# Optimization experiments

Measured on AMD Instinct MI355X. Metric: run time of the kernel, lower is better.

Reference implementation:

```python
import jax, jax.numpy as jnp
import numpy as np


def _fft_conv(x, filts):
    # x: [B, inC, S, S] real; filts: [inC, outC, k, k, 2] (real/imag channels)
    # Matches FFT_Conv_Layer: zero-pad bottom/right by k-1, FFT, complex
    # multiply-accumulate over inC, inverse FFT, crop [1:-1, 1:-1], take real.
    N = x.shape[-1] + filts.shape[-2] - 1  # imgSize + filtSize - 1
    Fx = jnp.fft.fft2(x, s=(N, N))                      # [B, inC, N, N] complex
    fc = filts[..., 0] + 1j * filts[..., 1]             # [inC, outC, k, k] complex
    Ff = jnp.fft.fft2(fc, s=(N, N))                     # [inC, outC, N, N]
    prod = jnp.einsum('bihw,iohw->bohw', Fx, Ff)        # sum over inC, no huge 5D temp
    return jnp.real(jnp.fft.ifft2(prod))[:, :, 1:-1, 1:-1]


def _spectral_pool(x, fsize):
    # Keep lowest `fsize` frequencies (corner crop of the FFT), inverse FFT, ReLU.
    F = jnp.fft.fft2(x)
    n = (fsize - 1) // 2
    tl = F[:, :, :n + 1, :n + 1]
    tr = F[:, :, :n + 1, -n:]
    bl = F[:, :, -n:, :n + 1]
    br = F[:, :, -n:, -n:]
    top = jnp.concatenate([tl, tr], axis=-1)
    bot = jnp.concatenate([bl, br], axis=-1)
    out = jnp.real(jnp.fft.ifft2(jnp.concatenate([top, bot], axis=-2)))
    return jax.nn.relu(out)


def setup_inputs() -> dict:
    key = jax.random.key(0)
    ks = jax.random.split(key, 10)
    B = 16
    filt_shapes = [(3, 32), (32, 64), (64, 128), (128, 256), (256, 256)]
    inp = {'x': jax.random.normal(ks[0], (B, 3, 224, 224), dtype=jnp.float32)}
    for i, (ci, co) in enumerate(filt_shapes):
        inp[f'f{i + 1}'] = 0.01 * jax.random.normal(ks[1 + i], (ci, co, 3, 3, 2), dtype=jnp.float32)
    inp['gamma'] = jnp.ones((256,), jnp.float32)
    inp['beta'] = jnp.zeros((256,), jnp.float32)
    inp['W1'] = 0.02 * jax.random.normal(ks[6], (9216, 512), dtype=jnp.float32)
    inp['b1'] = jnp.zeros((512,), jnp.float32)
    inp['W2'] = 0.02 * jax.random.normal(ks[7], (512, 256), dtype=jnp.float32)
    inp['b2'] = jnp.zeros((256,), jnp.float32)
    inp['W3'] = 0.02 * jax.random.normal(ks[8], (256, 10), dtype=jnp.float32)
    inp['b3'] = jnp.zeros((10,), jnp.float32)
    return inp


def reference(x, f1, f2, f3, f4, f5, gamma, beta, W1, b1, W2, b2, W3, b3):
    h = _spectral_pool(_fft_conv(x, f1), 113)   # [B, 32, 113, 113]
    h = _spectral_pool(_fft_conv(h, f2), 55)    # [B, 64, 55, 55]
    h = _spectral_pool(_fft_conv(h, f3), 27)    # [B, 128, 27, 27]
    h = _spectral_pool(_fft_conv(h, f4), 13)    # [B, 256, 13, 13]
    h = _fft_conv(h, f5)                        # [B, 256, 13, 13]
    # BatchNorm2d (training mode: batch statistics, biased variance)
    mean = jnp.mean(h, axis=(0, 2, 3), keepdims=True)
    var = jnp.var(h, axis=(0, 2, 3), keepdims=True)
    h = (h - mean) * jax.lax.rsqrt(var + 1e-5)
    h = h * gamma.reshape(1, -1, 1, 1) + beta.reshape(1, -1, 1, 1)
    # AdaptiveAvgPool2d((6,6)) on 13x13 == avg pool, kernel 3, stride 2
    h = jax.lax.reduce_window(h, 0.0, jax.lax.add, (1, 1, 3, 3), (1, 1, 2, 2), 'VALID') / 9.0
    h = h.reshape(h.shape[0], -1)               # [B, 9216]
    # dropout omitted (deterministic reference)
    h = jax.nn.relu(h @ W1 + b1)
    h = jax.nn.relu(h @ W2 + b2)
    return jax.nn.log_softmax(h @ W3 + b3, axis=1)
```

## Files before the change

### kernel.cpp

```cpp
#include <hip/hip_runtime.h>
#include <hip/hip_bf16.h>

typedef __attribute__((ext_vector_type(8))) short short8_t;
typedef __attribute__((ext_vector_type(4))) float float4_t;

#define OFF_CF  0u
#define OFF_PB1 25690112u
#define OFF_PB2 38765568u
#define OFF_PB3 44960768u
#define OFF_PB4 47946752u
#define OFF_C5  49331200u
#define OFF_AP  52100096u
#define OFF_H1  52689920u
#define OFF_H2  52722688u
#define OFF_P   52739072u
#define OFF_FPK 53918720u
#define OFF_PPK 55890944u

static __device__ __forceinline__ unsigned short f2bf(float v) {
    __hip_bfloat16 h = __float2bfloat16(v);
    return *(unsigned short*)&h;
}
static __device__ __forceinline__ float bf2f(unsigned short u) {
    __hip_bfloat16 h = *(__hip_bfloat16*)&u;
    return __bfloat162float(h);
}
static __device__ __forceinline__ unsigned short ld_bf(const float* p) { return f2bf(*p); }
static __device__ __forceinline__ unsigned short ld_bf(const unsigned short* p) { return *p; }
static __device__ __forceinline__ void st_out(float* p, float v) { *p = v; }
static __device__ __forceinline__ void st_out(unsigned short* p, float v) { *p = f2bf(v); }

__global__ void pack_f_k(const float* __restrict__ f, unsigned short* __restrict__ A,
                         int Ci, int Co, int CIR) {
    int id = blockIdx.x * 256 + threadIdx.x;
    int nci = Ci >> 5;
    int total = (Co >> 4) * nci * 9 * 512;
    if (id >= total) return;
    int j = id & 7, lane = (id >> 3) & 63;
    int uv = (id >> 9) % 9;
    int rest = id / (512 * 9);
    int cc = rest % nci, co_blk = rest / nci;
    int m = lane & 15, k = ((lane >> 4) << 3) + j;
    int ci = (cc << 5) + k, co = (co_blk << 4) + m;
    float v = (ci < CIR) ? f[((size_t)(ci * Co + co) * 9 + uv) * 2] : 0.f;
    A[id] = f2bf(v);
}

__global__ void pack_pool_k(unsigned short* __restrict__ P, int M, int N, int RT, int KC) {
    int id = blockIdx.x * 256 + threadIdx.x;
    if (id >= RT * KC * 512) return;
    int j = id & 7, lane = (id >> 3) & 63;
    int c = (id >> 9) % KC, rt = id / (512 * KC);
    int row = (rt << 4) + (lane & 15);
    int col = (c << 5) + ((lane >> 4) << 3) + j;
    double val = 0.0;
    if (row < M && col < N) {
        int n = (M - 1) / 2;
        double w = 6.283185307179586476925286766559 *
                   ((double)row / (double)M - (double)col / (double)N);
        double acc = 1.0;
        for (int a = 1; a <= n; ++a) acc += 2.0 * cos(w * (double)a);
        val = acc / (double)M;
    }
    float vf = (float)val;
    unsigned short hi = f2bf(vf);
    unsigned short lo = f2bf(vf - bf2f(hi));
    size_t base = ((size_t)(rt * KC + c) * 2) * 512 + lane * 8 + j;
    P[base] = hi;
    P[base + 512] = lo;
}

template<int CI, int CIR, int CO, int COB, int PBLK, int WQT, typename Tin, typename Tout>
__global__ __launch_bounds__(256) void conv_mfma2_k(const Tin* __restrict__ x,
        const unsigned short* __restrict__ Apk, Tout* __restrict__ y, int H) {
    constexpr int ROWS = PBLK + 2;
    constexpr int QW = WQT * 16 + 2;
    constexpr int RC = ROWS * QW;
    constexpr int NCC = CI >> 5;
    constexpr int NCOG = CO / COB;
    constexpr int NC = (WQT == 2) ? (COB / 32) : (COB / 64);
    __shared__ unsigned short xs[RC * 40];
    int b = blockIdx.z / NCOG;
    int co0 = (blockIdx.z % NCOG) * COB;
    int q0 = blockIdx.x * (WQT * 16);
    int p0 = blockIdx.y * PBLK;
    int tid = threadIdx.x;
    int lane = tid & 63, w = tid >> 6;
    int l15 = lane & 15;
    int kch = lane >> 4;
    int mg = kch << 2;
    int qt = (WQT == 2) ? (w & 1) : 0;
    int ctb = (WQT == 2) ? ((w >> 1) * NC) : (w * NC);
    const Tin* xb = x + (size_t)b * CIR * H * H;
    float4_t acc[PBLK][NC];
#pragma unroll
    for (int pr = 0; pr < PBLK; ++pr)
#pragma unroll
        for (int nc = 0; nc < NC; ++nc) acc[pr][nc] = (float4_t){0.f, 0.f, 0.f, 0.f};
    for (int cc = 0; cc < NCC; ++cc) {
        for (int i = tid; i < RC * 32; i += 256) {
            int ci = i / RC;
            int rc = i - ci * RC;
            int r = rc / QW;
            int c = rc - r * QW;
            int gp = p0 - 1 + r, gq = q0 - 1 + c;
            unsigned short v = 0;
            if ((CI == CIR || ((cc << 5) + ci) < CIR) &&
                (unsigned)gp < (unsigned)H && (unsigned)gq < (unsigned)H)
                v = ld_bf(&xb[((size_t)((cc << 5) + ci) * H + gp) * H + gq]);
            xs[rc * 40 + ((((ci >> 3) ^ ((rc >> 3) & 3)) << 3) | (ci & 7))] = v;
        }
        __syncthreads();
#pragma unroll
        for (int uv = 0; uv < 9; ++uv) {
            const int u = uv / 3, v = uv % 3;
            short8_t af[NC];
#pragma unroll
            for (int nc = 0; nc < NC; ++nc) {
                int ct = (co0 >> 4) + ctb + nc;
                af[nc] = *(const short8_t*)(Apk +
                    (((size_t)ct * NCC + cc) * 9 + uv) * 512 + lane * 8);
            }
#pragma unroll
            for (int pr = 0; pr < PBLK; ++pr) {
                int rcL = (pr + 2 - u) * QW + qt * 16 + (2 - v) + l15;
                int addr = rcL * 40 + ((kch ^ ((rcL >> 3) & 3)) << 3);
                short8_t bf = *(const short8_t*)(&xs[addr]);
#pragma unroll
                for (int nc = 0; nc < NC; ++nc)
                    acc[pr][nc] = __builtin_amdgcn_mfma_f32_16x16x32_bf16(
                        af[nc], bf, acc[pr][nc], 0, 0, 0);
            }
        }
        __syncthreads();
    }
    int q = q0 + qt * 16 + l15;
    if (q < H) {
#pragma unroll
        for (int pr = 0; pr < PBLK; ++pr) {
            int p = p0 + pr;
            if (p < H) {
#pragma unroll
                for (int nc = 0; nc < NC; ++nc) {
                    Tout* yb = y + (((size_t)b * CO + co0 + (ctb + nc) * 16 + mg) * H + p) * H + q;
#pragma unroll
                    for (int r2 = 0; r2 < 4; ++r2)
                        st_out(&yb[(size_t)r2 * H * H], acc[pr][nc][r2]);
                }
            }
        }
    }
}

template<int N, int M, int TRT>
__global__ __launch_bounds__(256) void pool_mfma_k(const float* __restrict__ x,
                                                   const unsigned short* __restrict__ PK,
                                                   unsigned short* __restrict__ out) {
    constexpr int MT = (N + 15) / 16;
    constexpr int RT = (M + 15) / 16;
    constexpr int KC = (N + 31) / 32;
    constexpr int XPAD = 40;
    constexpr int ZPAD = KC * 32 + 8;
    constexpr int XROWS = MT * 16;
    constexpr int NT1 = MT * TRT;
    constexpr int L1 = (NT1 + 3) / 4;
    constexpr int NT2 = RT * TRT;
    constexpr int L2 = (NT2 + 3) / 4;
    __shared__ unsigned short xh[XROWS * XPAD], xl[XROWS * XPAD];
    __shared__ unsigned short zh[16 * TRT * ZPAD], zl[16 * TRT * ZPAD];

    int t0g = blockIdx.x * TRT;
    int bc = blockIdx.y;
    int tid = threadIdx.x;
    int lane = tid & 63, w = tid >> 6;
    int l15 = lane & 15;
    int kb = (lane >> 4) << 3;
    const float* xb = x + (size_t)bc * N * N;

    float4_t acc[L1];
#pragma unroll
    for (int i = 0; i < L1; ++i) acc[i] = (float4_t){0.f, 0.f, 0.f, 0.f};

    for (int c = 0; c < KC; ++c) {
        for (int id = tid; id < XROWS * 32; id += 256) {
            int u = id >> 5, vv = id & 31, v = (c << 5) + vv;
            float val = (u < N && v < N) ? xb[u * N + v] : 0.f;
            unsigned short hi = f2bf(val);
            xh[u * XPAD + vv] = hi;
            xl[u * XPAD + vv] = f2bf(val - bf2f(hi));
        }
        __syncthreads();
#pragma unroll
        for (int li = 0; li < L1; ++li) {
            int idx = li * 4 + w;
            if (idx < NT1) {
                int mt = idx / TRT, nt = idx % TRT;
                short8_t ahi = *(const short8_t*)(&xh[(mt * 16 + l15) * XPAD + kb]);
                short8_t alo = *(const short8_t*)(&xl[(mt * 16 + l15) * XPAD + kb]);
                const unsigned short* bp =
                    PK + ((size_t)((t0g + nt) * KC + c) * 2) * 512 + lane * 8;
                short8_t bhi = *(const short8_t*)bp;
                short8_t blo = *(const short8_t*)(bp + 512);
                acc[li] = __builtin_amdgcn_mfma_f32_16x16x32_bf16(ahi, bhi, acc[li], 0, 0, 0);
                acc[li] = __builtin_amdgcn_mfma_f32_16x16x32_bf16(ahi, blo, acc[li], 0, 0, 0);
                acc[li] = __builtin_amdgcn_mfma_f32_16x16x32_bf16(alo, bhi, acc[li], 0, 0, 0);
            }
        }
        __syncthreads();
    }
#pragma unroll
    for (int li = 0; li < L1; ++li) {
        int idx = li * 4 + w;
        if (idx < NT1) {
            int mt = idx / TRT, nt = idx % TRT;
            int t = nt * 16 + l15;
            int u0 = mt * 16 + ((lane >> 4) << 2);
            unsigned short h0 = f2bf(acc[li][0]), h1 = f2bf(acc[li][1]);
            unsigned short h2 = f2bf(acc[li][2]), h3 = f2bf(acc[li][3]);
            unsigned long long ph =
                (unsigned long long)h0 | ((unsigned long long)h1 << 16) |
                ((unsigned long long)h2 << 32) | ((unsigned long long)h3 << 48);
            unsigned long long pl =
                (unsigned long long)f2bf(acc[li][0] - bf2f(h0)) |
                ((unsigned long long)f2bf(acc[li][1] - bf2f(h1)) << 16) |
                ((unsigned long long)f2bf(acc[li][2] - bf2f(h2)) << 32) |
                ((unsigned long long)f2bf(acc[li][3] - bf2f(h3)) << 48);
            *(unsigned long long*)(&zh[t * ZPAD + u0]) = ph;
            *(unsigned long long*)(&zl[t * ZPAD + u0]) = pl;
        }
    }
    __syncthreads();

    float4_t acc2[L2];
#pragma unroll
    for (int i = 0; i < L2; ++i) acc2[i] = (float4_t){0.f, 0.f, 0.f, 0.f};
    for (int c = 0; c < KC; ++c) {
#pragma unroll
        for (int li = 0; li < L2; ++li) {
            int idx = li * 4 + w;
            if (idx < NT2) {
                int mt = idx / TRT, nt = idx % TRT;
                const unsigned short* ap =
                    PK + ((size_t)(mt * KC + c) * 2) * 512 + lane * 8;
                short8_t ahi = *(const short8_t*)ap;
                short8_t alo = *(const short8_t*)(ap + 512);
                short8_t bzh = *(const short8_t*)(&zh[(nt * 16 + l15) * ZPAD + (c << 5) + kb]);
                short8_t bzl = *(const short8_t*)(&zl[(nt * 16 + l15) * ZPAD + (c << 5) + kb]);
                acc2[li] = __builtin_amdgcn_mfma_f32_16x16x32_bf16(ahi, bzh, acc2[li], 0, 0, 0);
                acc2[li] = __builtin_amdgcn_mfma_f32_16x16x32_bf16(ahi, bzl, acc2[li], 0, 0, 0);
                acc2[li] = __builtin_amdgcn_mfma_f32_16x16x32_bf16(alo, bzh, acc2[li], 0, 0, 0);
            }
        }
    }
    unsigned short* ob = out + (size_t)bc * M * M;
#pragma unroll
    for (int li = 0; li < L2; ++li) {
        int idx = li * 4 + w;
        if (idx < NT2) {
            int mt = idx / TRT, nt = idx % TRT;
            int t = (t0g + nt) * 16 + l15;
            if (t < M) {
                int s0 = mt * 16 + ((lane >> 4) << 2);
#pragma unroll
                for (int r = 0; r < 4; ++r) {
                    int s = s0 + r;
                    if (s < M) ob[s * M + t] = f2bf(fmaxf(acc2[li][r], 0.f));
                }
            }
        }
    }
}

__global__ void bn_k(float* __restrict__ h, const float* __restrict__ gamma,
                     const float* __restrict__ beta) {
    int c = blockIdx.x;
    int tid = threadIdx.x;
    float s = 0.f, s2 = 0.f;
    for (int i = tid; i < 16 * 169; i += 256) {
        int b = i / 169, hw = i % 169;
        float v = h[((size_t)b * 256 + c) * 169 + hw];
        s += v; s2 += v * v;
    }
    __shared__ float red[256], red2[256];
    red[tid] = s; red2[tid] = s2;
    __syncthreads();
    for (int st = 128; st > 0; st >>= 1) {
        if (tid < st) { red[tid] += red[tid + st]; red2[tid] += red2[tid + st]; }
        __syncthreads();
    }
    __shared__ float sc, sh;
    if (tid == 0) {
        float mean = red[0] / (16.f * 169.f);
        float var  = red2[0] / (16.f * 169.f) - mean * mean;
        float inv  = rsqrtf(var + 1e-5f);
        sc = gamma[c] * inv;
        sh = beta[c] - mean * sc;
    }
    __syncthreads();
    for (int i = tid; i < 16 * 169; i += 256) {
        int b = i / 169, hw = i % 169;
        size_t idx = ((size_t)b * 256 + c) * 169 + hw;
        h[idx] = h[idx] * sc + sh;
    }
}

__global__ void avgpool_k(const float* __restrict__ h, float* __restrict__ ap) {
    int id = blockIdx.x * 256 + threadIdx.x;
    if (id >= 16 * 256 * 36) return;
    int j = id % 6, i = (id / 6) % 6, c = (id / 36) % 256, b = id / (36 * 256);
    const float* hb = h + ((size_t)b * 256 + c) * 169;
    float s = 0.f;
#pragma unroll
    for (int di = 0; di < 3; ++di)
#pragma unroll
        for (int dj = 0; dj < 3; ++dj)
            s += hb[(2 * i + di) * 13 + (2 * j + dj)];
    ap[(size_t)b * 9216 + c * 36 + i * 6 + j] = s * (1.f / 9.f);
}

template<int BATCH, int KLEN>
__global__ void fc_part_k(const float* __restrict__ h, const float* __restrict__ W,
                          float* __restrict__ P, int Kdim, int N) {
    __shared__ float hs[BATCH * KLEN];
    __shared__ float red[BATCH * 64];
    int tx = threadIdx.x, ty = threadIdx.y;
    int tid = ty * 64 + tx;
    int o = blockIdx.x * 64 + tx;
    int k0 = blockIdx.y * KLEN;
    for (int i = tid; i < BATCH * KLEN; i += 256) {
        int b = i / KLEN, k = i % KLEN;
        hs[i] = h[(size_t)b * Kdim + k0 + k];
    }
    __syncthreads();
    float acc[BATCH];
#pragma unroll
    for (int b = 0; b < BATCH; ++b) acc[b] = 0.f;
    for (int k = ty; k < KLEN; k += 4) {
        float w = W[(size_t)(k0 + k) * N + o];
#pragma unroll
        for (int b = 0; b < BATCH; ++b) acc[b] += hs[b * KLEN + k] * w;
    }
    for (int kz = 0; kz < 4; ++kz) {
        if (ty == kz) {
#pragma unroll
            for (int b = 0; b < BATCH; ++b) {
                if (kz == 0) red[b * 64 + tx] = acc[b];
                else         red[b * 64 + tx] += acc[b];
            }
        }
        __syncthreads();
    }
    if (ty == 0) {
#pragma unroll
        for (int b = 0; b < BATCH; ++b)
            P[((size_t)blockIdx.y * BATCH + b) * N + o] = red[b * 64 + tx];
    }
}

template<int BATCH>
__global__ void fc_reduce_k(const float* __restrict__ P, const float* __restrict__ bias,
                            float* __restrict__ out, int N, int KS, int relu) {
    int id = blockIdx.x * 256 + threadIdx.x;
    if (id >= BATCH * N) return;
    int b = id / N, o = id % N;
    float s = bias[o];
    for (int ks = 0; ks < KS; ++ks) s += P[((size_t)ks * BATCH + b) * N + o];
    if (relu) s = fmaxf(s, 0.f);
    out[(size_t)b * N + o] = s;
}

__global__ void fc3_softmax_k(const float* __restrict__ h, const float* __restrict__ W,
                              const float* __restrict__ bias, float* __restrict__ out) {
    int b = blockIdx.x;
    int o = threadIdx.x;
    __shared__ float l[10];
    if (o < 10) {
        float acc = bias[o];
        for (int k = 0; k < 256; ++k) acc += h[b * 256 + k] * W[k * 10 + o];
        l[o] = acc;
    }
    __syncthreads();
    if (o == 0) {
        float m = l[0];
        for (int i = 1; i < 10; ++i) m = fmaxf(m, l[i]);
        float s = 0.f;
        for (int i = 0; i < 10; ++i) s += expf(l[i] - m);
        float lse = m + logf(s);
        for (int i = 0; i < 10; ++i) out[b * 10 + i] = l[i] - lse;
    }
}

extern "C" void kernel_launch(void* const* d_in, const int* in_sizes, int n_in,
                              void* d_out, int out_size, void* d_ws, size_t ws_size,
                              hipStream_t stream) {
    const float* x     = (const float*)d_in[0];
    const float* f1    = (const float*)d_in[1];
    const float* f2    = (const float*)d_in[2];
    const float* f3    = (const float*)d_in[3];
    const float* f4    = (const float*)d_in[4];
    const float* f5    = (const float*)d_in[5];
    const float* gamma = (const float*)d_in[6];
    const float* beta  = (const float*)d_in[7];
    const float* W1    = (const float*)d_in[8];
    const float* b1    = (const float*)d_in[9];
    const float* W2    = (const float*)d_in[10];
    const float* b2    = (const float*)d_in[11];
    const float* W3    = (const float*)d_in[12];
    const float* b3    = (const float*)d_in[13];
    float* out = (float*)d_out;
    char* ws = (char*)d_ws;

    float* CF = (float*)(ws + OFF_CF);
    unsigned short* PB1 = (unsigned short*)(ws + OFF_PB1);
    unsigned short* PB2 = (unsigned short*)(ws + OFF_PB2);
    unsigned short* PB3 = (unsigned short*)(ws + OFF_PB3);
    unsigned short* PB4 = (unsigned short*)(ws + OFF_PB4);
    float* C5 = (float*)(ws + OFF_C5);
    float* AP = (float*)(ws + OFF_AP);
    float* H1 = (float*)(ws + OFF_H1);
    float* H2 = (float*)(ws + OFF_H2);
    float* P  = (float*)(ws + OFF_P);
    unsigned short* PK1 = (unsigned short*)(ws + OFF_FPK);
    unsigned short* PK2 = PK1 + 9216;
    unsigned short* PK3 = PK2 + 18432;
    unsigned short* PK4 = PK3 + 73728;
    unsigned short* PK5 = PK4 + 294912;
    unsigned short* PP1 = (unsigned short*)(ws + OFF_PPK);
    unsigned short* PP2 = PP1 + 57344;
    unsigned short* PP3 = PP2 + 16384;
    unsigned short* PP4 = PP3 + 4096;

    pack_f_k<<<36,   256, 0, stream>>>(f1, PK1, 32, 32, 3);
    pack_f_k<<<72,   256, 0, stream>>>(f2, PK2, 32, 64, 32);
    pack_f_k<<<288,  256, 0, stream>>>(f3, PK3, 64, 128, 64);
    pack_f_k<<<1152, 256, 0, stream>>>(f4, PK4, 128, 256, 128);
    pack_f_k<<<2304, 256, 0, stream>>>(f5, PK5, 256, 256, 256);
    pack_pool_k<<<(8 * 7 * 512 + 255) / 256, 256, 0, stream>>>(PP1, 113, 224, 8, 7);
    pack_pool_k<<<(4 * 4 * 512 + 255) / 256, 256, 0, stream>>>(PP2, 55, 113, 4, 4);
    pack_pool_k<<<(2 * 2 * 512 + 255) / 256, 256, 0, stream>>>(PP3, 27, 55, 2, 2);
    pack_pool_k<<<(1 * 1 * 512 + 255) / 256, 256, 0, stream>>>(PP4, 13, 27, 1, 1);

    for (int ck = 0; ck < 4; ++ck) {
        int b0 = ck * 4;
        conv_mfma2_k<32, 3, 32, 32, 6, 2, float, float>
            <<<dim3(7, 38, 4), 256, 0, stream>>>(x + (size_t)b0 * 3 * 224 * 224, PK1, CF, 224);
        pool_mfma_k<224, 113, 4><<<dim3(2, 4 * 32), 256, 0, stream>>>(
            CF, PP1, PB1 + (size_t)b0 * 32 * 113 * 113);
    }
    for (int ck = 0; ck < 4; ++ck) {
        int b0 = ck * 4;
        conv_mfma2_k<32, 32, 64, 64, 6, 2, unsigned short, float>
            <<<dim3(4, 19, 4), 256, 0, stream>>>(PB1 + (size_t)b0 * 32 * 113 * 113, PK2, CF, 113);
        pool_mfma_k<113, 55, 4><<<dim3(1, 4 * 64), 256, 0, stream>>>(
            CF, PP2, PB2 + (size_t)b0 * 64 * 55 * 55);
    }
    conv_mfma2_k<64, 64, 128, 128, 6, 2, unsigned short, float>
        <<<dim3(2, 10, 16), 256, 0, stream>>>(PB2, PK3, CF, 55);
    pool_mfma_k<55, 27, 2><<<dim3(1, 16 * 128), 256, 0, stream>>>(CF, PP3, PB3);
    conv_mfma2_k<128, 128, 256, 128, 4, 2, unsigned short, float>
        <<<dim3(1, 7, 32), 256, 0, stream>>>(PB3, PK4, CF, 27);
    pool_mfma_k<27, 13, 1><<<dim3(1, 16 * 256), 256, 0, stream>>>(CF, PP4, PB4);
    conv_mfma2_k<256, 256, 256, 128, 2, 1, unsigned short, float>
        <<<dim3(1, 7, 32), 256, 0, stream>>>(PB4, PK5, C5, 13);

    bn_k<<<256, 256, 0, stream>>>(C5, gamma, beta);
    avgpool_k<<<(16 * 256 * 36 + 255) / 256, 256, 0, stream>>>(C5, AP);
    fc_part_k<16, 256><<<dim3(512 / 64, 36), dim3(64, 4), 0, stream>>>(AP, W1, P, 9216, 512);
    fc_reduce_k<16><<<(16 * 512 + 255) / 256, 256, 0, stream>>>(P, b1, H1, 512, 36, 1);
    fc_part_k<16, 64><<<dim3(256 / 64, 8), dim3(64, 4), 0, stream>>>(H1, W2, P, 512, 256);
    fc_reduce_k<16><<<(16 * 256 + 255) / 256, 256, 0, stream>>>(P, b2, H2, 256, 8, 1);
    fc3_softmax_k<<<16, 64, 0, stream>>>(H2, W3, b3, out);
}
```

Baseline: 777.7 us.

## Vectorize conv input staging with padded row strides and merge small kernels

```diff
diff --git a/kernel.cpp b/kernel.cpp
--- a/kernel.cpp
+++ b/kernel.cpp
@@ -5,17 +5,17 @@
 typedef __attribute__((ext_vector_type(4))) float float4_t;
 
 #define OFF_CF  0u
-#define OFF_PB1 25690112u
-#define OFF_PB2 38765568u
-#define OFF_PB3 44960768u
-#define OFF_PB4 47946752u
-#define OFF_C5  49331200u
-#define OFF_AP  52100096u
-#define OFF_H1  52689920u
-#define OFF_H2  52722688u
-#define OFF_P   52739072u
-#define OFF_FPK 53918720u
-#define OFF_PPK 55890944u
+#define OFF_PB1 26214400u
+#define OFF_PB2 40099840u
+#define OFF_PB3 46407680u
+#define OFF_PB4 49946624u
+#define OFF_C5  51650560u
+#define OFF_AP  54419456u
+#define OFF_H1  55009280u
+#define OFF_H2  55042048u
+#define OFF_P   55058432u
+#define OFF_FPK 56238080u
+#define OFF_PPK 58210304u
 
 static __device__ __forceinline__ unsigned short f2bf(float v) {
     __hip_bfloat16 h = __float2bfloat16(v);
@@ -27,15 +27,21 @@
 }
 static __device__ __forceinline__ unsigned short ld_bf(const float* p) { return f2bf(*p); }
 static __device__ __forceinline__ unsigned short ld_bf(const unsigned short* p) { return *p; }
-static __device__ __forceinline__ void st_out(float* p, float v) { *p = v; }
-static __device__ __forceinline__ void st_out(unsigned short* p, float v) { *p = f2bf(v); }
-
-__global__ void pack_f_k(const float* __restrict__ f, unsigned short* __restrict__ A,
-                         int Ci, int Co, int CIR) {
-    int id = blockIdx.x * 256 + threadIdx.x;
+
+__global__ void pack_f_all(const float* f1, const float* f2, const float* f3,
+                           const float* f4, const float* f5,
+                           unsigned short* A1, unsigned short* A2, unsigned short* A3,
+                           unsigned short* A4, unsigned short* A5) {
+    int bx = blockIdx.x;
+    const float* f; unsigned short* A; int Ci, Co, CIR, base;
+    if (bx < 36)        { f = f1; A = A1; Ci = 32;  Co = 32;  CIR = 3;   base = 0; }
+    else if (bx < 108)  { f = f2; A = A2; Ci = 32;  Co = 64;  CIR = 32;  base = 36; }
+    else if (bx < 396)  { f = f3; A = A3; Ci = 64;  Co = 128; CIR = 64;  base = 108; }
+    else if (bx < 1548) { f = f4; A = A4; Ci = 128; Co = 256; CIR = 128; base = 396; }
+    else                { f = f5; A = A5; Ci = 256; Co = 256; CIR = 256; base = 1548; }
+    int id = (bx - base) * 256 + threadIdx.x;
     int nci = Ci >> 5;
-    int total = (Co >> 4) * nci * 9 * 512;
-    if (id >= total) return;
+    if (id >= (Co >> 4) * nci * 9 * 512) return;
     int j = id & 7, lane = (id >> 3) & 63;
     int uv = (id >> 9) % 9;
     int rest = id / (512 * 9);
@@ -46,8 +52,16 @@
     A[id] = f2bf(v);
 }
 
-__global__ void pack_pool_k(unsigned short* __restrict__ P, int M, int N, int RT, int KC) {
-    int id = blockIdx.x * 256 + threadIdx.x;
+__global__ void pack_pool_all(unsigned short* P1, unsigned short* P2,
+                              unsigned short* P3, unsigned short* P4) {
+    int bx = blockIdx.x;
+    unsigned short* P; int M, N, KC, base;
+    if (bx < 112)      { P = P1; M = 113; N = 224; KC = 7; base = 0; }
+    else if (bx < 144) { P = P2; M = 55;  N = 113; KC = 4; base = 112; }
+    else if (bx < 152) { P = P3; M = 27;  N = 55;  KC = 2; base = 144; }
+    else               { P = P4; M = 13;  N = 27;  KC = 1; base = 152; }
+    int id = (bx - base) * 256 + threadIdx.x;
+    int RT = (M + 15) / 16;
     if (id >= RT * KC * 512) return;
     int j = id & 7, lane = (id >> 3) & 63;
     int c = (id >> 9) % KC, rt = id / (512 * KC);
@@ -65,16 +79,17 @@
     float vf = (float)val;
     unsigned short hi = f2bf(vf);
     unsigned short lo = f2bf(vf - bf2f(hi));
-    size_t base = ((size_t)(rt * KC + c) * 2) * 512 + lane * 8 + j;
-    P[base] = hi;
-    P[base + 512] = lo;
-}
-
-template<int CI, int CIR, int CO, int COB, int PBLK, int WQT, typename Tin, typename Tout>
-__global__ __launch_bounds__(256) void conv_mfma2_k(const Tin* __restrict__ x,
-        const unsigned short* __restrict__ Apk, Tout* __restrict__ y, int H) {
+    size_t bo = ((size_t)(rt * KC + c) * 2) * 512 + lane * 8 + j;
+    P[bo] = hi;
+    P[bo + 512] = lo;
+}
+
+template<int CI, int CIR, int CO, int COB, int PBLK, int WQT, typename Tin>
+__global__ __launch_bounds__(256) void conv_mfma3_k(const Tin* __restrict__ x,
+        const unsigned short* __restrict__ Apk, float* __restrict__ y, int H, int HS) {
     constexpr int ROWS = PBLK + 2;
     constexpr int QW = WQT * 16 + 2;
+    constexpr int QCH8 = (QW + 14) / 8;
     constexpr int RC = ROWS * QW;
     constexpr int NCC = CI >> 5;
     constexpr int NCOG = CO / COB;
@@ -91,24 +106,52 @@
     int mg = kch << 2;
     int qt = (WQT == 2) ? (w & 1) : 0;
     int ctb = (WQT == 2) ? ((w >> 1) * NC) : (w * NC);
-    const Tin* xb = x + (size_t)b * CIR * H * H;
+    const Tin* xb = x + (size_t)b * CIR * H * HS;
     float4_t acc[PBLK][NC];
 #pragma unroll
     for (int pr = 0; pr < PBLK; ++pr)
 #pragma unroll
         for (int nc = 0; nc < NC; ++nc) acc[pr][nc] = (float4_t){0.f, 0.f, 0.f, 0.f};
     for (int cc = 0; cc < NCC; ++cc) {
-        for (int i = tid; i < RC * 32; i += 256) {
-            int ci = i / RC;
-            int rc = i - ci * RC;
-            int r = rc / QW;
-            int c = rc - r * QW;
-            int gp = p0 - 1 + r, gq = q0 - 1 + c;
-            unsigned short v = 0;
-            if ((CI == CIR || ((cc << 5) + ci) < CIR) &&
-                (unsigned)gp < (unsigned)H && (unsigned)gq < (unsigned)H)
-                v = ld_bf(&xb[((size_t)((cc << 5) + ci) * H + gp) * H + gq]);
-            xs[rc * 40 + ((((ci >> 3) ^ ((rc >> 3) & 3)) << 3) | (ci & 7))] = v;
+        for (int i = tid; i < 32 * ROWS * QCH8; i += 256) {
+            int ci = i / (ROWS * QCH8);
+            int rem = i - ci * (ROWS * QCH8);
+            int r = rem / QCH8, ch = rem - r * QCH8;
+            int gci = (cc << 5) + ci;
+            int gp = p0 - 1 + r;
+            int gq0 = q0 - 8 + ch * 8;
+            bool rowok = (CI == CIR || gci < CIR) && ((unsigned)gp < (unsigned)H);
+            unsigned short vv[8];
+            if (rowok && ch >= 1 && ch * 8 <= QW - 1 && gq0 >= 0 && gq0 + 7 < H) {
+                const Tin* src = &xb[((size_t)gci * H + gp) * HS + gq0];
+                if constexpr (sizeof(Tin) == 2) {
+                    short8_t v8 = *(const short8_t*)src;
+#pragma unroll
+                    for (int j = 0; j < 8; ++j) vv[j] = (unsigned short)v8[j];
+                } else {
+                    float4_t f0 = *(const float4_t*)src;
+                    float4_t g0 = *(const float4_t*)(src + 4);
+#pragma unroll
+                    for (int j = 0; j < 4; ++j) { vv[j] = f2bf(f0[j]); vv[4 + j] = f2bf(g0[j]); }
+                }
+            } else {
+#pragma unroll
+                for (int j = 0; j < 8; ++j) {
+                    int gq = gq0 + j;
+                    unsigned short u = 0;
+                    if (rowok && (unsigned)gq < (unsigned)H)
+                        u = ld_bf(&xb[((size_t)gci * H + gp) * HS + gq]);
+                    vv[j] = u;
+                }
+            }
+#pragma unroll
+            for (int j = 0; j < 8; ++j) {
+                int c8 = ch * 8 + j - 7;
+                if ((unsigned)c8 < (unsigned)QW) {
+                    int rc = r * QW + c8;
+                    xs[rc * 40 + ((((ci >> 3) ^ ((rc >> 3) & 3)) << 3) | (ci & 7))] = vv[j];
+                }
+            }
         }
         __syncthreads();
 #pragma unroll
@@ -142,17 +185,17 @@
             if (p < H) {
 #pragma unroll
                 for (int nc = 0; nc < NC; ++nc) {
-                    Tout* yb = y + (((size_t)b * CO + co0 + (ctb + nc) * 16 + mg) * H + p) * H + q;
+                    float* yb = y + (((size_t)b * CO + co0 + (ctb + nc) * 16 + mg) * H + p) * H + q;
 #pragma unroll
                     for (int r2 = 0; r2 < 4; ++r2)
-                        st_out(&yb[(size_t)r2 * H * H], acc[pr][nc][r2]);
+                        yb[(size_t)r2 * H * H] = acc[pr][nc][r2];
                 }
             }
         }
     }
 }
 
-template<int N, int M, int TRT>
+template<int N, int M, int TRT, int MS>
 __global__ __launch_bounds__(256) void pool_mfma_k(const float* __restrict__ x,
                                                    const unsigned short* __restrict__ PK,
                                                    unsigned short* __restrict__ out) {
@@ -252,7 +295,7 @@
             }
         }
     }
-    unsigned short* ob = out + (size_t)bc * M * M;
+    unsigned short* ob = out + (size_t)bc * M * MS;
 #pragma unroll
     for (int li = 0; li < L2; ++li) {
         int idx = li * 4 + w;
@@ -264,24 +307,25 @@
 #pragma unroll
                 for (int r = 0; r < 4; ++r) {
                     int s = s0 + r;
-                    if (s < M) ob[s * M + t] = f2bf(fmaxf(acc2[li][r], 0.f));
+                    if (s < M) ob[s * MS + t] = f2bf(fmaxf(acc2[li][r], 0.f));
                 }
             }
         }
     }
 }
 
-__global__ void bn_k(float* __restrict__ h, const float* __restrict__ gamma,
-                     const float* __restrict__ beta) {
-    int c = blockIdx.x;
-    int tid = threadIdx.x;
+__global__ __launch_bounds__(256) void bn_avgpool_k(const float* __restrict__ h,
+        const float* __restrict__ gamma, const float* __restrict__ beta,
+        float* __restrict__ ap) {
+    int c = blockIdx.x, tid = threadIdx.x;
+    __shared__ float hs[16 * 169];
+    __shared__ float red[256], red2[256];
     float s = 0.f, s2 = 0.f;
     for (int i = tid; i < 16 * 169; i += 256) {
         int b = i / 169, hw = i % 169;
         float v = h[((size_t)b * 256 + c) * 169 + hw];
-        s += v; s2 += v * v;
-    }
-    __shared__ float red[256], red2[256];
+        hs[i] = v; s += v; s2 += v * v;
+    }
     red[tid] = s; red2[tid] = s2;
     __syncthreads();
     for (int st = 128; st > 0; st >>= 1) {
@@ -297,25 +341,17 @@
         sh = beta[c] - mean * sc;
     }
     __syncthreads();
-    for (int i = tid; i < 16 * 169; i += 256) {
-        int b = i / 169, hw = i % 169;
-        size_t idx = ((size_t)b * 256 + c) * 169 + hw;
-        h[idx] = h[idx] * sc + sh;
-    }
-}
-
-__global__ void avgpool_k(const float* __restrict__ h, float* __restrict__ ap) {
-    int id = blockIdx.x * 256 + threadIdx.x;
-    if (id >= 16 * 256 * 36) return;
-    int j = id % 6, i = (id / 6) % 6, c = (id / 36) % 256, b = id / (36 * 256);
-    const float* hb = h + ((size_t)b * 256 + c) * 169;
-    float s = 0.f;
-#pragma unroll
-    for (int di = 0; di < 3; ++di)
-#pragma unroll
-        for (int dj = 0; dj < 3; ++dj)
-            s += hb[(2 * i + di) * 13 + (2 * j + dj)];
-    ap[(size_t)b * 9216 + c * 36 + i * 6 + j] = s * (1.f / 9.f);
+    for (int i = tid; i < 16 * 36; i += 256) {
+        int b = i / 36, r = i % 36, ii = r / 6, jj = r % 6;
+        const float* hb = &hs[b * 169];
+        float sum = 0.f;
+#pragma unroll
+        for (int di = 0; di < 3; ++di)
+#pragma unroll
+            for (int dj = 0; dj < 3; ++dj)
+                sum += hb[(2 * ii + di) * 13 + 2 * jj + dj];
+        ap[(size_t)b * 9216 + c * 36 + r] = sum * (1.f / 9.f) * sc + sh;
+    }
 }
 
 template<int BATCH, int KLEN>
@@ -430,41 +466,33 @@
     unsigned short* PP3 = PP2 + 16384;
     unsigned short* PP4 = PP3 + 4096;
 
-    pack_f_k<<<36,   256, 0, stream>>>(f1, PK1, 32, 32, 3);
-    pack_f_k<<<72,   256, 0, stream>>>(f2, PK2, 32, 64, 32);
-    pack_f_k<<<288,  256, 0, stream>>>(f3, PK3, 64, 128, 64);
-    pack_f_k<<<1152, 256, 0, stream>>>(f4, PK4, 128, 256, 128);
-    pack_f_k<<<2304, 256, 0, stream>>>(f5, PK5, 256, 256, 256);
-    pack_pool_k<<<(8 * 7 * 512 + 255) / 256, 256, 0, stream>>>(PP1, 113, 224, 8, 7);
-    pack_pool_k<<<(4 * 4 * 512 + 255) / 256, 256, 0, stream>>>(PP2, 55, 113, 4, 4);
-    pack_pool_k<<<(2 * 2 * 512 + 255) / 256, 256, 0, stream>>>(PP3, 27, 55, 2, 2);
-    pack_pool_k<<<(1 * 1 * 512 + 255) / 256, 256, 0, stream>>>(PP4, 13, 27, 1, 1);
+    pack_f_all<<<3852, 256, 0, stream>>>(f1, f2, f3, f4, f5, PK1, PK2, PK3, PK4, PK5);
+    pack_pool_all<<<154, 256, 0, stream>>>(PP1, PP2, PP3, PP4);
 
     for (int ck = 0; ck < 4; ++ck) {
         int b0 = ck * 4;
-        conv_mfma2_k<32, 3, 32, 32, 6, 2, float, float>
-            <<<dim3(7, 38, 4), 256, 0, stream>>>(x + (size_t)b0 * 3 * 224 * 224, PK1, CF, 224);
-        pool_mfma_k<224, 113, 4><<<dim3(2, 4 * 32), 256, 0, stream>>>(
-            CF, PP1, PB1 + (size_t)b0 * 32 * 113 * 113);
-    }
-    for (int ck = 0; ck < 4; ++ck) {
-        int b0 = ck * 4;
-        conv_mfma2_k<32, 32, 64, 64, 6, 2, unsigned short, float>
-            <<<dim3(4, 19, 4), 256, 0, stream>>>(PB1 + (size_t)b0 * 32 * 113 * 113, PK2, CF, 113);
-        pool_mfma_k<113, 55, 4><<<dim3(1, 4 * 64), 256, 0, stream>>>(
-            CF, PP2, PB2 + (size_t)b0 * 64 * 55 * 55);
-    }
-    conv_mfma2_k<64, 64, 128, 128, 6, 2, unsigned short, float>
-        <<<dim3(2, 10, 16), 256, 0, stream>>>(PB2, PK3, CF, 55);
-    pool_mfma_k<55, 27, 2><<<dim3(1, 16 * 128), 256, 0, stream>>>(CF, PP3, PB3);
-    conv_mfma2_k<128, 128, 256, 128, 4, 2, unsigned short, float>
-        <<<dim3(1, 7, 32), 256, 0, stream>>>(PB3, PK4, CF, 27);
-    pool_mfma_k<27, 13, 1><<<dim3(1, 16 * 256), 256, 0, stream>>>(CF, PP4, PB4);
-    conv_mfma2_k<256, 256, 256, 128, 2, 1, unsigned short, float>
-        <<<dim3(1, 7, 32), 256, 0, stream>>>(PB4, PK5, C5, 13);
-
-    bn_k<<<256, 256, 0, stream>>>(C5, gamma, beta);
-    avgpool_k<<<(16 * 256 * 36 + 255) / 256, 256, 0, stream>>>(C5, AP);
+        conv_mfma3_k<32, 3, 32, 32, 6, 2, float>
+            <<<dim3(7, 38, 4), 256, 0, stream>>>(x + (size_t)b0 * 3 * 224 * 224, PK1, CF, 224, 224);
+        pool_mfma_k<224, 113, 4, 120><<<dim3(2, 4 * 32), 256, 0, stream>>>(
+            CF, PP1, PB1 + (size_t)b0 * 32 * 113 * 120);
+    }
+    for (int ck = 0; ck < 2; ++ck) {
+        int b0 = ck * 8;
+        conv_mfma3_k<32, 32, 64, 64, 6, 2, unsigned short>
+            <<<dim3(4, 19, 8), 256, 0, stream>>>(PB1 + (size_t)b0 * 32 * 113 * 120, PK2, CF, 113, 120);
+        pool_mfma_k<113, 55, 4, 56><<<dim3(1, 8 * 64), 256, 0, stream>>>(
+            CF, PP2, PB2 + (size_t)b0 * 64 * 55 * 56);
+    }
+    conv_mfma3_k<64, 64, 128, 64, 6, 2, unsigned short>
+        <<<dim3(2, 10, 32), 256, 0, stream>>>(PB2, PK3, CF, 55, 56);
+    pool_mfma_k<55, 27, 2, 32><<<dim3(1, 16 * 128), 256, 0, stream>>>(CF, PP3, PB3);
+    conv_mfma3_k<128, 128, 256, 64, 4, 2, unsigned short>
+        <<<dim3(1, 7, 64), 256, 0, stream>>>(PB3, PK4, CF, 27, 32);
+    pool_mfma_k<27, 13, 1, 16><<<dim3(1, 16 * 256), 256, 0, stream>>>(CF, PP4, PB4);
+    conv_mfma3_k<256, 256, 256, 64, 2, 1, unsigned short>
+        <<<dim3(1, 7, 64), 256, 0, stream>>>(PB4, PK5, C5, 13, 16);
+
+    bn_avgpool_k<<<256, 256, 0, stream>>>(C5, gamma, beta, AP);
     fc_part_k<16, 256><<<dim3(512 / 64, 36), dim3(64, 4), 0, stream>>>(AP, W1, P, 9216, 512);
     fc_reduce_k<16><<<(16 * 512 + 255) / 256, 256, 0, stream>>>(P, b1, H1, 512, 36, 1);
     fc_part_k<16, 64><<<dim3(256 / 64, 8), dim3(64, 4), 0, stream>>>(H1, W2, P, 512, 256);
```

Measured after the change: 631.3 us. -18.8%, faster.
